# Performance work log

Hardware: AMD Instinct MI355X
Metric: run time of the kernel (lower is better)

Reference implementation:

```python
import jax, jax.numpy as jnp
import numpy as np

N_STUDENT = 100000
N_ITEM = 20000
N_EDGES = 1000000
IN_CH = 128
EDGE_DIM = 32
DEC_CH = 64


def setup_inputs() -> dict:
    key = jax.random.key(0)
    ks = jax.random.split(key, 9)
    x_student = jax.random.normal(ks[0], (N_STUDENT, IN_CH), dtype=jnp.float32)
    x_item = jax.random.normal(ks[1], (N_ITEM, IN_CH), dtype=jnp.float32)
    edge_label_index = jax.random.randint(ks[2], (2, N_EDGES), 0, N_ITEM, dtype=jnp.int64)
    edge_feat = jax.random.normal(ks[3], (N_EDGES, EDGE_DIM), dtype=jnp.float32)
    offset = jax.random.normal(ks[4], (N_ITEM, 1), dtype=jnp.float32)
    # linear: (IN_CH + EDGE_DIM) -> DEC_CH ; linear_2: IN_CH -> DEC_CH
    s1 = 1.0 / np.sqrt(IN_CH + EDGE_DIM)
    s2 = 1.0 / np.sqrt(IN_CH)
    W1 = jax.random.uniform(ks[5], (IN_CH + EDGE_DIM, DEC_CH), minval=-s1, maxval=s1, dtype=jnp.float32)
    b1 = jax.random.uniform(ks[6], (DEC_CH,), minval=-s1, maxval=s1, dtype=jnp.float32)
    W2 = jax.random.uniform(ks[7], (IN_CH, DEC_CH), minval=-s2, maxval=s2, dtype=jnp.float32)
    b2 = jax.random.uniform(ks[8], (DEC_CH,), minval=-s2, maxval=s2, dtype=jnp.float32)
    return {
        "x_student": x_student, "x_item": x_item,
        "edge_label_index": edge_label_index, "edge_feat": edge_feat,
        "offset": offset, "W1": W1, "b1": b1, "W2": W2, "b2": b2,
    }


def reference(x_student, x_item, edge_label_index, edge_feat, offset, W1, b1, W2, b2):
    # Gather edge endpoints: [E, IN_CH]
    feat_s = x_student[edge_label_index[0]]
    feat_i = x_item[edge_label_index[1]]
    # x = elu(Linear(cat([feat_s, edge_feat])))  -> [E, DEC_CH]
    x = jnp.concatenate([feat_s, edge_feat], axis=-1)
    x = jax.nn.elu(x @ W1 + b1)
    # y = softplus(Linear_2(feat_i))  -> [E, DEC_CH]
    y = jax.nn.softplus(feat_i @ W2 + b2)
    # elementwise mult + sum reduce -> [E, 1]
    out = jnp.sum(x * y, axis=-1, keepdims=True)
    # offset gather by item index, add
    out = out + offset[edge_label_index[1]]
    return out
```

## Files before the change

### kernel.cpp

```cpp
#include <hip/hip_runtime.h>
#include <math.h>

#define N_STUDENT 100000
#define N_ITEM    20000
#define N_EDGES   1000000
#define IN_CH     128
#define EDGE_DIM  32
#define DEC_CH    64

#define N_ROWS    N_ITEM


typedef __attribute__((ext_vector_type(8))) short short8;
typedef __attribute__((ext_vector_type(4))) float f32x4;

__device__ __forceinline__ short bf16_rne(float f) {
    union { float f; unsigned u; } v; v.f = f;
    unsigned r = (v.u + 0x7FFFu + ((v.u >> 16) & 1u)) >> 16;
    return (short)r;
}

__device__ __forceinline__ short8 cvt8(float4 a0, float4 a1) {
    short8 s;
    s[0] = bf16_rne(a0.x); s[1] = bf16_rne(a0.y);
    s[2] = bf16_rne(a0.z); s[3] = bf16_rne(a0.w);
    s[4] = bf16_rne(a1.x); s[5] = bf16_rne(a1.y);
    s[6] = bf16_rne(a1.z); s[7] = bf16_rne(a1.w);
    return s;
}

#define PRE_BLOCKS 313

__global__ __launch_bounds__(256) void precompute_kernel(
    const float* __restrict__ x_student, const float* __restrict__ x_item,
    const float* __restrict__ W1, const float* __restrict__ b1,
    const float* __restrict__ W2, const float* __restrict__ b2,
    float* __restrict__ s_part, float* __restrict__ y_item)
{
    const int phase = (blockIdx.x >= PRE_BLOCKS);
    const int blk   = phase ? blockIdx.x - PRE_BLOCKS : blockIdx.x;
    const float* X  = phase ? x_item : x_student;
    const float* W  = phase ? W2 : W1;
    const float* B  = phase ? b2 : b1;
    float* OUT      = phase ? y_item : s_part;

    const int lane = threadIdx.x & 63;
    const int m = lane & 15, q = lane >> 4;
    const int wib = threadIdx.x >> 6;
    const int r0w = blk * 64 + wib * 16;
    if (r0w >= N_ROWS) return;

    short8 bfr[4][4];
    #pragma unroll
    for (int ks = 0; ks < 4; ++ks)
        #pragma unroll
        for (int ct = 0; ct < 4; ++ct)
            #pragma unroll
            for (int j = 0; j < 8; ++j)
                bfr[ks][ct][j] = bf16_rne(W[(ks * 32 + q * 8 + j) * DEC_CH + ct * 16 + m]);

    float bc[4];
    #pragma unroll
    for (int ct = 0; ct < 4; ++ct) bc[ct] = B[ct * 16 + m];

    int row = r0w + m;
    row = row < N_ROWS ? row : N_ROWS - 1;
    const float* xp = X + (size_t)row * IN_CH + q * 8;

    f32x4 acc[4];
    #pragma unroll
    for (int ct = 0; ct < 4; ++ct) acc[ct] = (f32x4){bc[ct], bc[ct], bc[ct], bc[ct]};

    #pragma unroll
    for (int ks = 0; ks < 4; ++ks) {
        float4 a0 = *(const float4*)(xp + ks * 32);
        float4 a1 = *(const float4*)(xp + ks * 32 + 4);
        short8 af = cvt8(a0, a1);
        #pragma unroll
        for (int ct = 0; ct < 4; ++ct)
            acc[ct] = __builtin_amdgcn_mfma_f32_16x16x32_bf16(af, bfr[ks][ct], acc[ct], 0, 0, 0);
    }

    #pragma unroll
    for (int reg = 0; reg < 4; ++reg) {
        const int orow = r0w + q * 4 + reg;
        if (orow < N_ROWS) {
            float4 fv;
            if (phase) {
                fv.x = fmaxf(acc[0][reg], 0.f) + log1pf(__expf(-fabsf(acc[0][reg])));
                fv.y = fmaxf(acc[1][reg], 0.f) + log1pf(__expf(-fabsf(acc[1][reg])));
                fv.z = fmaxf(acc[2][reg], 0.f) + log1pf(__expf(-fabsf(acc[2][reg])));
                fv.w = fmaxf(acc[3][reg], 0.f) + log1pf(__expf(-fabsf(acc[3][reg])));
            } else {
                fv.x = acc[0][reg]; fv.y = acc[1][reg];
                fv.z = acc[2][reg]; fv.w = acc[3][reg];
            }
            *(float4*)(OUT + (size_t)orow * DEC_CH + m * 4) = fv;
        }
    }
}

__global__ __launch_bounds__(256) void edge_kernel(
    const int* __restrict__ idx, const float* __restrict__ ef,
    const float* __restrict__ W1, const float* __restrict__ offset,
    const float* __restrict__ s_part, const float* __restrict__ y_item,
    float* __restrict__ out)
{
    __shared__ int2  sIdx[256];
    __shared__ float sOff[256];

    const int lane = threadIdx.x & 63;
    const int m = lane & 15, q = lane >> 4;
    const int e0 = blockIdx.x * 256;

    {
        const int t = threadIdx.x;
        if (e0 + t < N_EDGES) {
            const int is = idx[e0 + t];
            const int ii = idx[N_EDGES + e0 + t];
            sIdx[t] = make_int2(is, ii);
            sOff[t] = offset[ii];
        }
    }

    const float* Wb = W1 + IN_CH * DEC_CH;
    short8 bfr[4];
    #pragma unroll
    for (int ct = 0; ct < 4; ++ct)
        #pragma unroll
        for (int j = 0; j < 8; ++j)
            bfr[ct][j] = bf16_rne(Wb[(q * 8 + j) * DEC_CH + ct * 16 + m]);

    __syncthreads();

    const int wib = threadIdx.x >> 6;
    const int ew0 = e0 + wib * 64;
    if (ew0 >= N_EDGES) return;

    #pragma unroll
    for (int rt = 0; rt < 4; ++rt) {
        const float* ap = ef + (size_t)(ew0 + rt * 16 + m) * EDGE_DIM + q * 8;
        float4 a0 = *(const float4*)ap;
        float4 a1 = *(const float4*)(ap + 4);

        int2 ip[4];
        #pragma unroll
        for (int r = 0; r < 4; ++r)
            ip[r] = sIdx[wib * 64 + rt * 16 + q * 4 + r];

        float4 sg[4], yg[4];
        #pragma unroll
        for (int r = 0; r < 4; ++r) {
            sg[r] = *(const float4*)(s_part + (size_t)ip[r].x * DEC_CH + m * 4);
            yg[r] = *(const float4*)(y_item + (size_t)ip[r].y * DEC_CH + m * 4);
        }

        short8 af = cvt8(a0, a1);
        f32x4 acc[4];
        #pragma unroll
        for (int ct = 0; ct < 4; ++ct) {
            f32x4 z = {0.f, 0.f, 0.f, 0.f};
            acc[ct] = __builtin_amdgcn_mfma_f32_16x16x32_bf16(af, bfr[ct], z, 0, 0, 0);
        }

        float pr[4];
        #pragma unroll
        for (int r = 0; r < 4; ++r) {
            float t0 = acc[0][r] + sg[r].x;
            float t1 = acc[1][r] + sg[r].y;
            float t2 = acc[2][r] + sg[r].z;
            float t3 = acc[3][r] + sg[r].w;
            float x0 = t0 > 0.f ? t0 : (__expf(t0) - 1.f);
            float x1 = t1 > 0.f ? t1 : (__expf(t1) - 1.f);
            float x2 = t2 > 0.f ? t2 : (__expf(t2) - 1.f);
            float x3 = t3 > 0.f ? t3 : (__expf(t3) - 1.f);
            float p = x0 * yg[r].x;
            p = fmaf(x1, yg[r].y, p);
            p = fmaf(x2, yg[r].z, p);
            p = fmaf(x3, yg[r].w, p);
            pr[r] = p;
        }

        #pragma unroll
        for (int s = 1; s <= 8; s <<= 1) {
            pr[0] += __shfl_xor(pr[0], s, 64);
            pr[1] += __shfl_xor(pr[1], s, 64);
            pr[2] += __shfl_xor(pr[2], s, 64);
            pr[3] += __shfl_xor(pr[3], s, 64);
        }

        float v = (m & 3) == 0 ? pr[0]
                : (m & 3) == 1 ? pr[1]
                : (m & 3) == 2 ? pr[2] : pr[3];
        if (m < 4) {
            const int el = wib * 64 + rt * 16 + q * 4 + m;
            out[e0 + el] = v + sOff[el];
        }
    }
}

extern "C" void kernel_launch(void* const* d_in, const int* in_sizes, int n_in,
                              void* d_out, int out_size, void* d_ws, size_t ws_size,
                              hipStream_t stream) {
    const float* x_student = (const float*)d_in[0];
    const float* x_item    = (const float*)d_in[1];
    const int*   eli       = (const int*)d_in[2];
    const float* edge_feat = (const float*)d_in[3];
    const float* offset    = (const float*)d_in[4];
    const float* W1        = (const float*)d_in[5];
    const float* b1        = (const float*)d_in[6];
    const float* W2        = (const float*)d_in[7];
    const float* b2        = (const float*)d_in[8];
    float* out = (float*)d_out;

    float* s_part = (float*)d_ws;
    float* y_item = s_part + (size_t)N_ROWS * DEC_CH;

    precompute_kernel<<<2 * PRE_BLOCKS, 256, 0, stream>>>(
        x_student, x_item, W1, b1, W2, b2, s_part, y_item);
    edge_kernel<<<(N_EDGES + 255) / 256, 256, 0, stream>>>(
        eli, edge_feat, W1, offset, s_part, y_item, out);
}
```

Baseline: 277.3 us.

## Store per-node projection tables as packed bf16 and batch edge gathers

The precomputed per-row student and item projections are now stored as packed bf16 pairs instead of fp32, which halves the bytes read by the random gathers in the edge kernel. The edge kernel issues all loads for its four row tiles up front (edge features, both gathered tables, offsets) before any MFMA work, so more memory requests are in flight at once. The precompute kernel now handles two 16-row tiles per wave with half as many blocks. The cost is extra bf16 rounding of intermediates and higher register pressure in the edge kernel.

```diff
diff --git a/kernel.cpp b/kernel.cpp
--- a/kernel.cpp
+++ b/kernel.cpp
@@ -14,10 +14,16 @@
 typedef __attribute__((ext_vector_type(8))) short short8;
 typedef __attribute__((ext_vector_type(4))) float f32x4;
 
-__device__ __forceinline__ short bf16_rne(float f) {
+__device__ __forceinline__ unsigned bf16u(float f) {
     union { float f; unsigned u; } v; v.f = f;
-    unsigned r = (v.u + 0x7FFFu + ((v.u >> 16) & 1u)) >> 16;
-    return (short)r;
+    return (v.u + 0x7FFFu + ((v.u >> 16) & 1u)) >> 16;
+}
+__device__ __forceinline__ short bf16_rne(float f) { return (short)bf16u(f); }
+__device__ __forceinline__ float bflo(unsigned u) {
+    union { unsigned u; float f; } v; v.u = u << 16; return v.f;
+}
+__device__ __forceinline__ float bfhi(unsigned u) {
+    union { unsigned u; float f; } v; v.u = u & 0xffff0000u; return v.f;
 }
 
 __device__ __forceinline__ short8 cvt8(float4 a0, float4 a1) {
@@ -29,26 +35,26 @@
     return s;
 }
 
-#define PRE_BLOCKS 313
+#define PRE_BLOCKS 157
 
 __global__ __launch_bounds__(256) void precompute_kernel(
     const float* __restrict__ x_student, const float* __restrict__ x_item,
     const float* __restrict__ W1, const float* __restrict__ b1,
     const float* __restrict__ W2, const float* __restrict__ b2,
-    float* __restrict__ s_part, float* __restrict__ y_item)
+    unsigned* __restrict__ s_tab, unsigned* __restrict__ y_tab)
 {
     const int phase = (blockIdx.x >= PRE_BLOCKS);
     const int blk   = phase ? blockIdx.x - PRE_BLOCKS : blockIdx.x;
     const float* X  = phase ? x_item : x_student;
     const float* W  = phase ? W2 : W1;
     const float* B  = phase ? b2 : b1;
-    float* OUT      = phase ? y_item : s_part;
+    unsigned* OUT   = phase ? y_tab : s_tab;
 
     const int lane = threadIdx.x & 63;
     const int m = lane & 15, q = lane >> 4;
     const int wib = threadIdx.x >> 6;
-    const int r0w = blk * 64 + wib * 16;
-    if (r0w >= N_ROWS) return;
+    const int rbase = blk * 128 + wib * 32;
+    if (rbase >= N_ROWS) return;
 
     short8 bfr[4][4];
     #pragma unroll
@@ -63,39 +69,47 @@
     #pragma unroll
     for (int ct = 0; ct < 4; ++ct) bc[ct] = B[ct * 16 + m];
 
-    int row = r0w + m;
-    row = row < N_ROWS ? row : N_ROWS - 1;
-    const float* xp = X + (size_t)row * IN_CH + q * 8;
-
-    f32x4 acc[4];
-    #pragma unroll
-    for (int ct = 0; ct < 4; ++ct) acc[ct] = (f32x4){bc[ct], bc[ct], bc[ct], bc[ct]};
-
-    #pragma unroll
-    for (int ks = 0; ks < 4; ++ks) {
-        float4 a0 = *(const float4*)(xp + ks * 32);
-        float4 a1 = *(const float4*)(xp + ks * 32 + 4);
-        short8 af = cvt8(a0, a1);
+    #pragma unroll
+    for (int t = 0; t < 2; ++t) {
+        const int r0w = rbase + t * 16;
+        if (r0w >= N_ROWS) break;
+
+        int row = r0w + m;
+        row = row < N_ROWS ? row : N_ROWS - 1;
+        const float* xp = X + (size_t)row * IN_CH + q * 8;
+
+        f32x4 acc[4];
         #pragma unroll
         for (int ct = 0; ct < 4; ++ct)
-            acc[ct] = __builtin_amdgcn_mfma_f32_16x16x32_bf16(af, bfr[ks][ct], acc[ct], 0, 0, 0);
-    }
-
-    #pragma unroll
-    for (int reg = 0; reg < 4; ++reg) {
-        const int orow = r0w + q * 4 + reg;
-        if (orow < N_ROWS) {
-            float4 fv;
-            if (phase) {
-                fv.x = fmaxf(acc[0][reg], 0.f) + log1pf(__expf(-fabsf(acc[0][reg])));
-                fv.y = fmaxf(acc[1][reg], 0.f) + log1pf(__expf(-fabsf(acc[1][reg])));
-                fv.z = fmaxf(acc[2][reg], 0.f) + log1pf(__expf(-fabsf(acc[2][reg])));
-                fv.w = fmaxf(acc[3][reg], 0.f) + log1pf(__expf(-fabsf(acc[3][reg])));
-            } else {
-                fv.x = acc[0][reg]; fv.y = acc[1][reg];
-                fv.z = acc[2][reg]; fv.w = acc[3][reg];
+            acc[ct] = (f32x4){bc[ct], bc[ct], bc[ct], bc[ct]};
+
+        #pragma unroll
+        for (int ks = 0; ks < 4; ++ks) {
+            float4 a0 = *(const float4*)(xp + ks * 32);
+            float4 a1 = *(const float4*)(xp + ks * 32 + 4);
+            short8 af = cvt8(a0, a1);
+            #pragma unroll
+            for (int ct = 0; ct < 4; ++ct)
+                acc[ct] = __builtin_amdgcn_mfma_f32_16x16x32_bf16(af, bfr[ks][ct], acc[ct], 0, 0, 0);
+        }
+
+        #pragma unroll
+        for (int reg = 0; reg < 4; ++reg) {
+            const int orow = r0w + q * 4 + reg;
+            if (orow < N_ROWS) {
+                float v0 = acc[0][reg], v1 = acc[1][reg];
+                float v2 = acc[2][reg], v3 = acc[3][reg];
+                if (phase) {
+                    v0 = fmaxf(v0, 0.f) + log1pf(__expf(-fabsf(v0)));
+                    v1 = fmaxf(v1, 0.f) + log1pf(__expf(-fabsf(v1)));
+                    v2 = fmaxf(v2, 0.f) + log1pf(__expf(-fabsf(v2)));
+                    v3 = fmaxf(v3, 0.f) + log1pf(__expf(-fabsf(v3)));
+                }
+                uint2 pv;
+                pv.x = bf16u(v0) | (bf16u(v1) << 16);
+                pv.y = bf16u(v2) | (bf16u(v3) << 16);
+                *(uint2*)(OUT + (size_t)orow * 32 + m * 2) = pv;
             }
-            *(float4*)(OUT + (size_t)orow * DEC_CH + m * 4) = fv;
         }
     }
 }
@@ -103,11 +117,10 @@
 __global__ __launch_bounds__(256) void edge_kernel(
     const int* __restrict__ idx, const float* __restrict__ ef,
     const float* __restrict__ W1, const float* __restrict__ offset,
-    const float* __restrict__ s_part, const float* __restrict__ y_item,
+    const unsigned* __restrict__ s_tab, const unsigned* __restrict__ y_tab,
     float* __restrict__ out)
 {
-    __shared__ int2  sIdx[256];
-    __shared__ float sOff[256];
+    __shared__ int2 sIdx[256];
 
     const int lane = threadIdx.x & 63;
     const int m = lane & 15, q = lane >> 4;
@@ -119,7 +132,6 @@
             const int is = idx[e0 + t];
             const int ii = idx[N_EDGES + e0 + t];
             sIdx[t] = make_int2(is, ii);
-            sOff[t] = offset[ii];
         }
     }
 
@@ -137,25 +149,30 @@
     const int ew0 = e0 + wib * 64;
     if (ew0 >= N_EDGES) return;
 
+    float4 a0[4], a1[4];
+    int2   ip[4][4];
+    uint2  sg[4][4], yg[4][4];
+    float  offv[4];
+
     #pragma unroll
     for (int rt = 0; rt < 4; ++rt) {
         const float* ap = ef + (size_t)(ew0 + rt * 16 + m) * EDGE_DIM + q * 8;
-        float4 a0 = *(const float4*)ap;
-        float4 a1 = *(const float4*)(ap + 4);
-
-        int2 ip[4];
+        a0[rt] = *(const float4*)ap;
+        a1[rt] = *(const float4*)(ap + 4);
         #pragma unroll
         for (int r = 0; r < 4; ++r)
-            ip[r] = sIdx[wib * 64 + rt * 16 + q * 4 + r];
-
-        float4 sg[4], yg[4];
+            ip[rt][r] = sIdx[wib * 64 + rt * 16 + q * 4 + r];
         #pragma unroll
         for (int r = 0; r < 4; ++r) {
-            sg[r] = *(const float4*)(s_part + (size_t)ip[r].x * DEC_CH + m * 4);
-            yg[r] = *(const float4*)(y_item + (size_t)ip[r].y * DEC_CH + m * 4);
-        }
-
-        short8 af = cvt8(a0, a1);
+            sg[rt][r] = *(const uint2*)(s_tab + (size_t)ip[rt][r].x * 32 + m * 2);
+            yg[rt][r] = *(const uint2*)(y_tab + (size_t)ip[rt][r].y * 32 + m * 2);
+        }
+        offv[rt] = offset[ip[rt][m & 3].y];
+    }
+
+    #pragma unroll
+    for (int rt = 0; rt < 4; ++rt) {
+        short8 af = cvt8(a0[rt], a1[rt]);
         f32x4 acc[4];
         #pragma unroll
         for (int ct = 0; ct < 4; ++ct) {
@@ -166,18 +183,22 @@
         float pr[4];
         #pragma unroll
         for (int r = 0; r < 4; ++r) {
-            float t0 = acc[0][r] + sg[r].x;
-            float t1 = acc[1][r] + sg[r].y;
-            float t2 = acc[2][r] + sg[r].z;
-            float t3 = acc[3][r] + sg[r].w;
+            const float s0 = bflo(sg[rt][r].x), s1 = bfhi(sg[rt][r].x);
+            const float s2 = bflo(sg[rt][r].y), s3 = bfhi(sg[rt][r].y);
+            const float y0 = bflo(yg[rt][r].x), y1 = bfhi(yg[rt][r].x);
+            const float y2 = bflo(yg[rt][r].y), y3 = bfhi(yg[rt][r].y);
+            float t0 = acc[0][r] + s0;
+            float t1 = acc[1][r] + s1;
+            float t2 = acc[2][r] + s2;
+            float t3 = acc[3][r] + s3;
             float x0 = t0 > 0.f ? t0 : (__expf(t0) - 1.f);
             float x1 = t1 > 0.f ? t1 : (__expf(t1) - 1.f);
             float x2 = t2 > 0.f ? t2 : (__expf(t2) - 1.f);
             float x3 = t3 > 0.f ? t3 : (__expf(t3) - 1.f);
-            float p = x0 * yg[r].x;
-            p = fmaf(x1, yg[r].y, p);
-            p = fmaf(x2, yg[r].z, p);
-            p = fmaf(x3, yg[r].w, p);
+            float p = x0 * y0;
+            p = fmaf(x1, y1, p);
+            p = fmaf(x2, y2, p);
+            p = fmaf(x3, y3, p);
             pr[r] = p;
         }
 
@@ -192,10 +213,8 @@
         float v = (m & 3) == 0 ? pr[0]
                 : (m & 3) == 1 ? pr[1]
                 : (m & 3) == 2 ? pr[2] : pr[3];
-        if (m < 4) {
-            const int el = wib * 64 + rt * 16 + q * 4 + m;
-            out[e0 + el] = v + sOff[el];
-        }
+        if (m < 4)
+            out[ew0 + rt * 16 + q * 4 + m] = v + offv[rt];
     }
 }
 
@@ -213,11 +232,11 @@
     const float* b2        = (const float*)d_in[8];
     float* out = (float*)d_out;
 
-    float* s_part = (float*)d_ws;
-    float* y_item = s_part + (size_t)N_ROWS * DEC_CH;
+    unsigned* s_tab = (unsigned*)d_ws;
+    unsigned* y_tab = s_tab + (size_t)N_ROWS * 32;
 
     precompute_kernel<<<2 * PRE_BLOCKS, 256, 0, stream>>>(
-        x_student, x_item, W1, b1, W2, b2, s_part, y_item);
+        x_student, x_item, W1, b1, W2, b2, s_tab, y_tab);
     edge_kernel<<<(N_EDGES + 255) / 256, 256, 0, stream>>>(
-        eli, edge_feat, W1, offset, s_part, y_item, out);
-}
+        eli, edge_feat, W1, offset, s_tab, y_tab, out);
+}
```

Result: slower. 288.4 us (+4.0%).
